# Kernel optimization log

Hardware: AMD Instinct MI355X
Metric: run time of the kernel (lower is better)

The kernel has to match this reference:

```python
import jax, jax.numpy as jnp
import numpy as np

D_MODEL, N_HEADS, D_FF = 1024, 16, 2752
B, S = 2, 2048
EPS = 1e-5


def setup_inputs() -> dict:
    key = jax.random.key(0)
    ks = jax.random.split(key, 8)
    def w(k, fan_in, fan_out):
        std = np.sqrt(2.0 / (fan_in + fan_out))
        return jax.random.truncated_normal(k, -3.0, 3.0, (fan_in, fan_out), jnp.float32) * std
    return {
        "x": jax.random.normal(ks[0], (B, S, D_MODEL), jnp.float32),
        "g1": jnp.ones((D_MODEL,), jnp.float32),
        "g2": jnp.ones((D_MODEL,), jnp.float32),
        "w_q": w(ks[1], D_MODEL, D_MODEL),
        "w_k": w(ks[2], D_MODEL, D_MODEL),
        "w_v": w(ks[3], D_MODEL, D_MODEL),
        "w_o": w(ks[4], D_MODEL, D_MODEL),
        "w1": w(ks[5], D_MODEL, D_FF),
        "w2": w(ks[6], D_FF, D_MODEL),
        "w3": w(ks[7], D_MODEL, D_FF),
    }


def rmsnorm(x, g):
    xf = x.astype(jnp.float32)
    rms = jnp.sqrt(jnp.mean(xf * xf, axis=-1, keepdims=True) + EPS)
    return (xf / rms).astype(x.dtype) * g


def reference(x, g1, g2, w_q, w_k, w_v, w_o, w1, w2, w3):
    b, s, d = x.shape
    h = N_HEADS
    dh = d // h

    # --- causal multi-head self-attention on norm1(x) ---
    xn = rmsnorm(x, g1)
    q = (xn @ w_q).reshape(b, s, h, dh).transpose(0, 2, 1, 3)  # b h s d
    k = (xn @ w_k).reshape(b, s, h, dh).transpose(0, 2, 1, 3)
    v = (xn @ w_v).reshape(b, s, h, dh).transpose(0, 2, 1, 3)

    scores = jnp.einsum('bhqd,bhkd->bhqk', q, k) / jnp.sqrt(jnp.float32(dh))
    causal = jnp.tril(jnp.ones((s, s), dtype=bool))
    scores = jnp.where(causal, scores, -jnp.inf)
    probs = jax.nn.softmax(scores, axis=-1)
    attn = jnp.einsum('bhqk,bhkd->bhqd', probs, v)
    attn = attn.transpose(0, 2, 1, 3).reshape(b, s, d)
    h_res = x + attn @ w_o

    # --- SwiGLU FFN on norm2(h) ---
    hn = rmsnorm(h_res, g2)
    x1 = hn @ w1
    gate = x1 * jax.nn.sigmoid(x1)
    ffn = (gate * (hn @ w3)) @ w2
    return h_res + ffn
```

## Files before the change

kernel.cpp:

```cpp
#include <hip/hip_runtime.h>
#include <hip/hip_bf16.h>

typedef unsigned short u16;
typedef __bf16 bf16x8 __attribute__((ext_vector_type(8)));
typedef float  f32x4  __attribute__((ext_vector_type(4)));

#define D_MODEL 1024
#define SEQ     2048
#define NHEAD   16
#define DHEAD   64
#define QKVS    3072

__device__ __forceinline__ float bflo(unsigned u) { return __uint_as_float(u << 16); }
__device__ __forceinline__ float bfhi(unsigned u) { return __uint_as_float(u & 0xffff0000u); }
__device__ __forceinline__ u16 f2bf(float f) {
    unsigned u = __float_as_uint(f);
    u += 0x7fffu + ((u >> 16) & 1u);
    return (u16)(u >> 16);
}
__device__ __forceinline__ void gld_lds16(const u16* g, u16* l) {
    __builtin_amdgcn_global_load_lds((const __attribute__((address_space(1))) void*)g,
                                     (__attribute__((address_space(3))) void*)l, 16, 0, 0);
}

__global__ void detect_k(const unsigned* __restrict__ g1w, int* __restrict__ flag) {
    int c = 0;
#pragma unroll
    for (int i = 0; i < 8; ++i) c += (g1w[i] == 0x3F800000u) ? 1 : 0;
    *flag = (c >= 4) ? 1 : 0;
}

__global__ __launch_bounds__(256) void tp_k(const void* __restrict__ in_, u16* __restrict__ out,
                                            int K, int N, const int* __restrict__ flagp) {
    __shared__ u16 tile[32][33];
    const int f32 = *flagp;
    int k0 = blockIdx.x * 32, n0 = blockIdx.y * 32;
    int tx = threadIdx.x & 31, ty = threadIdx.x >> 5;
#pragma unroll
    for (int i = 0; i < 32; i += 8) {
        int nn = n0 + tx;
        u16 v = 0;
        if (nn < N) {
            size_t idx = (size_t)(k0 + ty + i) * N + nn;
            v = f32 ? f2bf(((const float*)in_)[idx]) : ((const u16*)in_)[idx];
        }
        tile[ty + i][tx] = v;
    }
    __syncthreads();
#pragma unroll
    for (int i = 0; i < 32; i += 8)
        out[(size_t)(n0 + ty + i) * K + (k0 + tx)] = tile[tx][ty + i];
}

__global__ __launch_bounds__(256) void rms_k(const void* __restrict__ x_, const void* __restrict__ g_,
                                             u16* __restrict__ o, const int* __restrict__ flagp,
                                             int x_raw) {
    const size_t row = blockIdx.x;
    const int f32 = *flagp;
    const int xf32 = f32 & x_raw;
    int t = threadIdx.x;
    float f0, f1, f2, f3, g0, g1, g2, g3;
    if (xf32) {
        float4 xv = *(const float4*)((const float*)x_ + row * D_MODEL + t * 4);
        f0 = xv.x; f1 = xv.y; f2 = xv.z; f3 = xv.w;
    } else {
        uint2 u = *(const uint2*)((const u16*)x_ + row * D_MODEL + t * 4);
        f0 = bflo(u.x); f1 = bfhi(u.x); f2 = bflo(u.y); f3 = bfhi(u.y);
    }
    if (f32) {
        float4 gv = *(const float4*)((const float*)g_ + t * 4);
        g0 = gv.x; g1 = gv.y; g2 = gv.z; g3 = gv.w;
    } else {
        uint2 gu = *(const uint2*)((const u16*)g_ + t * 4);
        g0 = bflo(gu.x); g1 = bfhi(gu.x); g2 = bflo(gu.y); g3 = bfhi(gu.y);
    }
    float s = f0 * f0 + f1 * f1 + f2 * f2 + f3 * f3;
#pragma unroll
    for (int off = 32; off > 0; off >>= 1) s += __shfl_xor(s, off, 64);
    __shared__ float ps[4];
    if ((t & 63) == 0) ps[t >> 6] = s;
    __syncthreads();
    float tot = ps[0] + ps[1] + ps[2] + ps[3];
    float rinv = rsqrtf(tot * (1.0f / D_MODEL) + 1e-5f);
    float fv[4] = {f0, f1, f2, f3};
    float gv2[4] = {g0, g1, g2, g3};
    u16 r[4];
#pragma unroll
    for (int i = 0; i < 4; ++i)
        r[i] = f2bf(fv[i] * rinv * gv2[i]);
    uint2 w;
    w.x = (unsigned)r[0] | ((unsigned)r[1] << 16);
    w.y = (unsigned)r[2] | ((unsigned)r[3] << 16);
    *(uint2*)(o + row * D_MODEL + t * 4) = w;
}

__global__ __launch_bounds__(256) void gemm_k(const u16* __restrict__ A, int lda,
                                              const u16* __restrict__ Bt, int ldb,
                                              u16* C, int ldc,
                                              const void* res, int K, int mode,
                                              const int* __restrict__ flagp, int res_raw,
                                              int out32) {
    __shared__ alignas(16) u16 As[128 * 32];
    __shared__ alignas(16) u16 Bs[128 * 32];
    const int t = threadIdx.x;
    const int rf32 = (mode == 1 && res_raw) ? *flagp : 0;
    const int wid = t >> 6, lane = t & 63;
    const int wm = (wid >> 1) * 64, wn = (wid & 1) * 64;
    const int m0 = blockIdx.x * 128, n0 = blockIdx.y * 128;
    const int fr = lane & 15, quad = lane >> 4;

    f32x4 acc[4][4] = {};

    for (int k0 = 0; k0 < K; k0 += 32) {
        __syncthreads();
#pragma unroll
        for (int r = 0; r < 2; ++r) {
            int e = r * 256 + t;
            int row = e >> 2, c = (e & 3) * 8;
            gld_lds16(A  + (size_t)(m0 + row) * lda + k0 + c, As + e * 8);
            gld_lds16(Bt + (size_t)(n0 + row) * ldb + k0 + c, Bs + e * 8);
        }
        __syncthreads();
        bf16x8 af[4], bfr[4];
#pragma unroll
        for (int i = 0; i < 4; ++i) {
            af[i]  = *(const bf16x8*)(As + (wm + i * 16 + fr) * 32 + quad * 8);
            bfr[i] = *(const bf16x8*)(Bs + (wn + i * 16 + fr) * 32 + quad * 8);
        }
#pragma unroll
        for (int i = 0; i < 4; ++i)
#pragma unroll
            for (int j = 0; j < 4; ++j)
                acc[i][j] = __builtin_amdgcn_mfma_f32_16x16x32_bf16(af[i], bfr[j], acc[i][j], 0, 0, 0);
    }

#pragma unroll
    for (int i = 0; i < 4; ++i)
#pragma unroll
        for (int j = 0; j < 4; ++j)
#pragma unroll
            for (int r2 = 0; r2 < 4; ++r2) {
                int row = m0 + wm + i * 16 + quad * 4 + r2;
                int col = n0 + wn + j * 16 + fr;
                size_t idx = (size_t)row * ldc + col;
                float v = acc[i][j][r2];
                if (mode == 1) {
                    float rv = rf32 ? ((const float*)res)[idx]
                                    : __uint_as_float((unsigned)((const u16*)res)[idx] << 16);
                    v += rv;
                } else if (mode == 2) {
                    float xv = __uint_as_float((unsigned)((const u16*)res)[idx] << 16);
                    xv = fminf(fmaxf(xv, -60.f), 60.f);
                    float sg = xv / (1.0f + __expf(-xv));
                    v = sg * v;
                }
                if (out32) ((float*)C)[idx] = v;
                else       C[idx] = f2bf(v);
            }
}

__global__ __launch_bounds__(256) void vtp_k(const u16* __restrict__ qkv, u16* __restrict__ vt) {
    __shared__ u16 tile[32][33];
    const int bh = blockIdx.z, b = bh >> 4, h = bh & 15;
    const int s0 = blockIdx.x * 32, d0 = blockIdx.y * 32;
    const int tx = threadIdx.x & 31, ty = threadIdx.x >> 5;
#pragma unroll
    for (int i = 0; i < 32; i += 8)
        tile[ty + i][tx] = qkv[(size_t)(b * SEQ + s0 + ty + i) * QKVS + 2048 + h * 64 + d0 + tx];
    __syncthreads();
#pragma unroll
    for (int i = 0; i < 32; i += 8)
        vt[(size_t)(bh * 64 + d0 + ty + i) * SEQ + s0 + tx] = tile[tx][ty + i];
}

#define KPAD 68
#define PPAD 72
__global__ __launch_bounds__(256) void fattn_k(const u16* __restrict__ QKV, const u16* __restrict__ Vt,
                                               u16* __restrict__ O) {
    __shared__ alignas(16) u16 Ks[64 * KPAD];
    __shared__ alignas(16) u16 Vs[64 * KPAD];
    __shared__ alignas(16) u16 Ps[4 * 16 * PPAD];

    const int bh = blockIdx.y;
    const size_t baseqk = ((size_t)(bh >> 4) * SEQ) * QKVS + (size_t)(bh & 15) * DHEAD;
    const size_t baseo  = ((size_t)(bh >> 4) * SEQ) * D_MODEL + (size_t)(bh & 15) * DHEAD;
    const size_t vtbase = (size_t)bh * 64 * SEQ;
    const u16* Qp = QKV + baseqk;
    const u16* Kp = QKV + baseqk + 1024;
    const int chunk = (gridDim.x - 1) - blockIdx.x;
    const int r0 = chunk * 64;
    const int t = threadIdx.x, w = t >> 6, lane = t & 63;
    const int fr = lane & 15, quad = lane >> 4;

    bf16x8 qa[2];
    {
        const u16* qp = Qp + (size_t)(r0 + w * 16 + fr) * QKVS + quad * 8;
        qa[0] = *(const bf16x8*)(qp);
        qa[1] = *(const bf16x8*)(qp + 32);
    }

    f32x4 oacc[4] = {};
    float lp[4] = {};
    u16* Pw = Ps + w * 16 * PPAD;
    const float sc = 0.125f * 1.44269504f;
    const int qrow_base = r0 + w * 16 + quad * 4;

    const int kend = r0 + 64;
    for (int kb = 0; kb < kend; kb += 64) {
        __syncthreads();
#pragma unroll
        for (int it = 0; it < 2; ++it) {
            int e = it * 256 + t;
            int rr = e >> 3, cc = (e & 7) * 8;
            *(uint4*)(Ks + rr * KPAD + cc) = *(const uint4*)(Kp + (size_t)(kb + rr) * QKVS + cc);
            *(uint4*)(Vs + rr * KPAD + cc) = *(const uint4*)(Vt + vtbase + (size_t)rr * SEQ + kb + cc);
        }
        __syncthreads();

        f32x4 sac[4] = {};
#pragma unroll
        for (int n = 0; n < 4; ++n) {
            bf16x8 kf0 = *(const bf16x8*)(Ks + (n * 16 + fr) * KPAD + quad * 8);
            bf16x8 kf1 = *(const bf16x8*)(Ks + (n * 16 + fr) * KPAD + 32 + quad * 8);
            sac[n] = __builtin_amdgcn_mfma_f32_16x16x32_bf16(qa[0], kf0, sac[n], 0, 0, 0);
            sac[n] = __builtin_amdgcn_mfma_f32_16x16x32_bf16(qa[1], kf1, sac[n], 0, 0, 0);
        }
        bf16x8 vf[8];
#pragma unroll
        for (int n = 0; n < 4; ++n) {
            vf[2 * n]     = *(const bf16x8*)(Vs + (n * 16 + fr) * KPAD + quad * 8);
            vf[2 * n + 1] = *(const bf16x8*)(Vs + (n * 16 + fr) * KPAD + 32 + quad * 8);
        }
#pragma unroll
        for (int n = 0; n < 4; ++n) {
            int key = kb + n * 16 + fr;
#pragma unroll
            for (int r = 0; r < 4; ++r) {
                float s = fminf(sac[n][r] * sc, 126.f);
                float p = (key <= qrow_base + r) ? exp2f(s) : 0.f;
                lp[r] += p;
                Pw[(quad * 4 + r) * PPAD + n * 16 + fr] = f2bf(p);
            }
        }
        __threadfence_block();
        bf16x8 pa0 = *(const bf16x8*)(Pw + fr * PPAD + quad * 8);
        bf16x8 pa1 = *(const bf16x8*)(Pw + fr * PPAD + 32 + quad * 8);
#pragma unroll
        for (int n = 0; n < 4; ++n) {
            oacc[n] = __builtin_amdgcn_mfma_f32_16x16x32_bf16(pa0, vf[2 * n],     oacc[n], 0, 0, 0);
            oacc[n] = __builtin_amdgcn_mfma_f32_16x16x32_bf16(pa1, vf[2 * n + 1], oacc[n], 0, 0, 0);
        }
    }

#pragma unroll
    for (int r = 0; r < 4; ++r) {
        float v = lp[r];
        v += __shfl_xor(v, 1, 64);
        v += __shfl_xor(v, 2, 64);
        v += __shfl_xor(v, 4, 64);
        v += __shfl_xor(v, 8, 64);
        lp[r] = 1.0f / v;
    }
#pragma unroll
    for (int r = 0; r < 4; ++r) {
        u16* op = O + baseo + (size_t)(qrow_base + r) * D_MODEL;
#pragma unroll
        for (int n = 0; n < 4; ++n)
            op[n * 16 + fr] = f2bf(oacc[n][r] * lp[r]);
    }
}

extern "C" void kernel_launch(void* const* d_in, const int* in_sizes, int n_in,
                              void* d_out, int out_size, void* d_ws, size_t ws_size,
                              hipStream_t stream) {
    const void* x  = d_in[0];
    const void* g1 = d_in[1];
    const void* g2 = d_in[2];
    const void* wq = d_in[3];
    const void* wk = d_in[4];
    const void* wv = d_in[5];
    const void* wo = d_in[6];
    const void* w1 = d_in[7];
    const void* w2 = d_in[8];
    const void* w3 = d_in[9];
    u16* ws  = (u16*)d_ws;

    u16* xn    = ws;
    u16* qkv   = ws + 4194304;
    u16* x1    = ws + 4194304;
    u16* hres  = ws + 16777216;
    int* flag  = (int*)(ws + 20971520);
    u16* wqkvT = ws + 20971776;
    u16* woT   = ws + 20971776;
    u16* w2T   = ws + 20971776;
    u16* vt    = (u16*)d_out;
    u16* attn  = (u16*)d_out + 4194304;
    u16* w1T   = (u16*)d_out;
    u16* w3T   = (u16*)d_out + 2883584;

    detect_k<<<1, 1, 0, stream>>>((const unsigned*)g1, flag);

    tp_k<<<dim3(32, 32), 256, 0, stream>>>(wq, wqkvT,               1024, 1024, flag);
    tp_k<<<dim3(32, 32), 256, 0, stream>>>(wk, wqkvT + 1048576,     1024, 1024, flag);
    tp_k<<<dim3(32, 32), 256, 0, stream>>>(wv, wqkvT + 2097152,     1024, 1024, flag);
    rms_k<<<4096, 256, 0, stream>>>(x, g1, xn, flag, 1);

    gemm_k<<<dim3(32, 24), 256, 0, stream>>>(xn, 1024, wqkvT, 1024, qkv, QKVS, nullptr, 1024, 0, flag, 0, 0);

    tp_k<<<dim3(32, 32), 256, 0, stream>>>(wo, woT, 1024, 1024, flag);
    vtp_k<<<dim3(64, 2, 32), 256, 0, stream>>>(qkv, vt);
    fattn_k<<<dim3(32, 32), 256, 0, stream>>>(qkv, vt, attn);

    gemm_k<<<dim3(32, 8), 256, 0, stream>>>(attn, 1024, woT, 1024, hres, 1024, x, 1024, 1, flag, 1, 0);

    rms_k<<<4096, 256, 0, stream>>>(hres, g2, xn, flag, 0);

    tp_k<<<dim3(32, 88), 256, 0, stream>>>(w1, w1T, 1024, 2752, flag);
    tp_k<<<dim3(32, 88), 256, 0, stream>>>(w3, w3T, 1024, 2752, flag);
    tp_k<<<dim3(86, 32), 256, 0, stream>>>(w2, w2T, 2752, 1024, flag);

    gemm_k<<<dim3(32, 22), 256, 0, stream>>>(xn, 1024, w1T, 1024, x1, 2816, nullptr, 1024, 0, flag, 0, 0);
    gemm_k<<<dim3(32, 22), 256, 0, stream>>>(xn, 1024, w3T, 1024, x1, 2816, x1, 1024, 2, flag, 0, 0);

    gemm_k<<<dim3(32, 8), 256, 0, stream>>>(x1, 2816, w2T, 2752, (u16*)d_out, 1024, hres, 2752, 1, flag, 0, 1);
}
```

Before: 520.6 us.

## Fuse W1/W3 GEMMs into one SwiGLU kernel and double-buffer attention K/V

Replaces the two FFN GEMM launches (W1, then W3 with SiLU gating in the epilogue) with a single ffn_k kernel. It loads the xn tile once, accumulates both products, and writes the gated result directly, which removes the intermediate x1 write and re-read. The flash attention kernel now double-buffers K/V tiles, prefetching the next block into registers during compute, and skips causal masking on fully unmasked blocks. It also switches P rounding to a cheaper round-half-up conversion. The fused kernel holds two 64-accumulator sets, which raises register pressure, and the attention kernel now uses more LDS.

```diff
diff --git a/kernel.cpp b/kernel.cpp
--- a/kernel.cpp
+++ b/kernel.cpp
@@ -17,6 +17,9 @@
     unsigned u = __float_as_uint(f);
     u += 0x7fffu + ((u >> 16) & 1u);
     return (u16)(u >> 16);
+}
+__device__ __forceinline__ u16 f2bf_fast(float f) {
+    return (u16)((__float_as_uint(f) + 0x8000u) >> 16);
 }
 __device__ __forceinline__ void gld_lds16(const u16* g, u16* l) {
     __builtin_amdgcn_global_load_lds((const __attribute__((address_space(1))) void*)g,
@@ -148,14 +151,67 @@
                     float rv = rf32 ? ((const float*)res)[idx]
                                     : __uint_as_float((unsigned)((const u16*)res)[idx] << 16);
                     v += rv;
-                } else if (mode == 2) {
-                    float xv = __uint_as_float((unsigned)((const u16*)res)[idx] << 16);
-                    xv = fminf(fmaxf(xv, -60.f), 60.f);
-                    float sg = xv / (1.0f + __expf(-xv));
-                    v = sg * v;
                 }
                 if (out32) ((float*)C)[idx] = v;
                 else       C[idx] = f2bf(v);
+            }
+}
+
+__global__ __launch_bounds__(256, 2) void ffn_k(const u16* __restrict__ A,
+                                                const u16* __restrict__ B1t,
+                                                const u16* __restrict__ B3t,
+                                                u16* __restrict__ G, int ldg) {
+    __shared__ alignas(16) u16 As[128 * 32];
+    __shared__ alignas(16) u16 B1s[128 * 32];
+    __shared__ alignas(16) u16 B3s[128 * 32];
+    const int t = threadIdx.x;
+    const int wid = t >> 6, lane = t & 63;
+    const int wm = (wid >> 1) * 64, wn = (wid & 1) * 64;
+    const int m0 = blockIdx.x * 128, n0 = blockIdx.y * 128;
+    const int fr = lane & 15, quad = lane >> 4;
+
+    f32x4 acc1[4][4] = {};
+    f32x4 acc3[4][4] = {};
+
+    for (int k0 = 0; k0 < 1024; k0 += 32) {
+        __syncthreads();
+#pragma unroll
+        for (int r = 0; r < 2; ++r) {
+            int e = r * 256 + t;
+            int row = e >> 2, c = (e & 3) * 8;
+            gld_lds16(A   + (size_t)(m0 + row) * 1024 + k0 + c, As  + e * 8);
+            gld_lds16(B1t + (size_t)(n0 + row) * 1024 + k0 + c, B1s + e * 8);
+            gld_lds16(B3t + (size_t)(n0 + row) * 1024 + k0 + c, B3s + e * 8);
+        }
+        __syncthreads();
+        bf16x8 af[4], b1[4], b3[4];
+#pragma unroll
+        for (int i = 0; i < 4; ++i) {
+            af[i] = *(const bf16x8*)(As  + (wm + i * 16 + fr) * 32 + quad * 8);
+            b1[i] = *(const bf16x8*)(B1s + (wn + i * 16 + fr) * 32 + quad * 8);
+            b3[i] = *(const bf16x8*)(B3s + (wn + i * 16 + fr) * 32 + quad * 8);
+        }
+#pragma unroll
+        for (int i = 0; i < 4; ++i)
+#pragma unroll
+            for (int j = 0; j < 4; ++j) {
+                acc1[i][j] = __builtin_amdgcn_mfma_f32_16x16x32_bf16(af[i], b1[j], acc1[i][j], 0, 0, 0);
+                acc3[i][j] = __builtin_amdgcn_mfma_f32_16x16x32_bf16(af[i], b3[j], acc3[i][j], 0, 0, 0);
+            }
+    }
+
+#pragma unroll
+    for (int i = 0; i < 4; ++i)
+#pragma unroll
+        for (int j = 0; j < 4; ++j)
+#pragma unroll
+            for (int r2 = 0; r2 < 4; ++r2) {
+                int row = m0 + wm + i * 16 + quad * 4 + r2;
+                int col = n0 + wn + j * 16 + fr;
+                float xv = acc1[i][j][r2];
+                xv = fminf(fmaxf(xv, -60.f), 60.f);
+                float sg = xv / (1.0f + __expf(-xv));
+                G[(size_t)row * ldg + col] = f2bf(sg * acc3[i][j][r2]);
             }
 }
 
@@ -177,8 +233,8 @@
 #define PPAD 72
 __global__ __launch_bounds__(256) void fattn_k(const u16* __restrict__ QKV, const u16* __restrict__ Vt,
                                                u16* __restrict__ O) {
-    __shared__ alignas(16) u16 Ks[64 * KPAD];
-    __shared__ alignas(16) u16 Vs[64 * KPAD];
+    __shared__ alignas(16) u16 Ks[2][64 * KPAD];
+    __shared__ alignas(16) u16 Vs[2][64 * KPAD];
     __shared__ alignas(16) u16 Ps[4 * 16 * PPAD];
 
     const int bh = blockIdx.y;
@@ -191,6 +247,8 @@
     const int r0 = chunk * 64;
     const int t = threadIdx.x, w = t >> 6, lane = t & 63;
     const int fr = lane & 15, quad = lane >> 4;
+    const int rr0 = t >> 3, cc0 = (t & 7) * 8;
+    const int rr1 = rr0 + 32;
 
     bf16x8 qa[2];
     {
@@ -203,43 +261,63 @@
     float lp[4] = {};
     u16* Pw = Ps + w * 16 * PPAD;
     const float sc = 0.125f * 1.44269504f;
-    const int qrow_base = r0 + w * 16 + quad * 4;
-
+    const int qrow_min  = r0 + w * 16;
+    const int qrow_base = qrow_min + quad * 4;
     const int kend = r0 + 64;
-    for (int kb = 0; kb < kend; kb += 64) {
-        __syncthreads();
-#pragma unroll
-        for (int it = 0; it < 2; ++it) {
-            int e = it * 256 + t;
-            int rr = e >> 3, cc = (e & 7) * 8;
-            *(uint4*)(Ks + rr * KPAD + cc) = *(const uint4*)(Kp + (size_t)(kb + rr) * QKVS + cc);
-            *(uint4*)(Vs + rr * KPAD + cc) = *(const uint4*)(Vt + vtbase + (size_t)rr * SEQ + kb + cc);
-        }
-        __syncthreads();
-
+
+    {
+        uint4 k0v = *(const uint4*)(Kp + (size_t)rr0 * QKVS + cc0);
+        uint4 k1v = *(const uint4*)(Kp + (size_t)rr1 * QKVS + cc0);
+        uint4 v0v = *(const uint4*)(Vt + vtbase + (size_t)rr0 * SEQ + cc0);
+        uint4 v1v = *(const uint4*)(Vt + vtbase + (size_t)rr1 * SEQ + cc0);
+        *(uint4*)(Ks[0] + rr0 * KPAD + cc0) = k0v;
+        *(uint4*)(Ks[0] + rr1 * KPAD + cc0) = k1v;
+        *(uint4*)(Vs[0] + rr0 * KPAD + cc0) = v0v;
+        *(uint4*)(Vs[0] + rr1 * KPAD + cc0) = v1v;
+    }
+    __syncthreads();
+
+    int cur = 0;
+    for (int kb = 0; kb < kend; kb += 64, cur ^= 1) {
+        const int nxt = kb + 64;
+        const bool have = nxt < kend;
+        uint4 kn0, kn1, vn0, vn1;
+        if (have) {
+            kn0 = *(const uint4*)(Kp + (size_t)(nxt + rr0) * QKVS + cc0);
+            kn1 = *(const uint4*)(Kp + (size_t)(nxt + rr1) * QKVS + cc0);
+            vn0 = *(const uint4*)(Vt + vtbase + (size_t)rr0 * SEQ + nxt + cc0);
+            vn1 = *(const uint4*)(Vt + vtbase + (size_t)rr1 * SEQ + nxt + cc0);
+        }
+
+        const u16* Kc = Ks[cur];
+        const u16* Vc = Vs[cur];
         f32x4 sac[4] = {};
 #pragma unroll
         for (int n = 0; n < 4; ++n) {
-            bf16x8 kf0 = *(const bf16x8*)(Ks + (n * 16 + fr) * KPAD + quad * 8);
-            bf16x8 kf1 = *(const bf16x8*)(Ks + (n * 16 + fr) * KPAD + 32 + quad * 8);
+            bf16x8 kf0 = *(const bf16x8*)(Kc + (n * 16 + fr) * KPAD + quad * 8);
+            bf16x8 kf1 = *(const bf16x8*)(Kc + (n * 16 + fr) * KPAD + 32 + quad * 8);
             sac[n] = __builtin_amdgcn_mfma_f32_16x16x32_bf16(qa[0], kf0, sac[n], 0, 0, 0);
             sac[n] = __builtin_amdgcn_mfma_f32_16x16x32_bf16(qa[1], kf1, sac[n], 0, 0, 0);
         }
-        bf16x8 vf[8];
-#pragma unroll
-        for (int n = 0; n < 4; ++n) {
-            vf[2 * n]     = *(const bf16x8*)(Vs + (n * 16 + fr) * KPAD + quad * 8);
-            vf[2 * n + 1] = *(const bf16x8*)(Vs + (n * 16 + fr) * KPAD + 32 + quad * 8);
-        }
-#pragma unroll
-        for (int n = 0; n < 4; ++n) {
-            int key = kb + n * 16 + fr;
-#pragma unroll
-            for (int r = 0; r < 4; ++r) {
-                float s = fminf(sac[n][r] * sc, 126.f);
-                float p = (key <= qrow_base + r) ? exp2f(s) : 0.f;
-                lp[r] += p;
-                Pw[(quad * 4 + r) * PPAD + n * 16 + fr] = f2bf(p);
+        if (nxt <= qrow_min) {
+#pragma unroll
+            for (int n = 0; n < 4; ++n)
+#pragma unroll
+                for (int r = 0; r < 4; ++r) {
+                    float p = exp2f(fminf(sac[n][r] * sc, 126.f));
+                    lp[r] += p;
+                    Pw[(quad * 4 + r) * PPAD + n * 16 + fr] = f2bf_fast(p);
+                }
+        } else {
+#pragma unroll
+            for (int n = 0; n < 4; ++n) {
+                int key = kb + n * 16 + fr;
+#pragma unroll
+                for (int r = 0; r < 4; ++r) {
+                    float p = (key <= qrow_base + r) ? exp2f(fminf(sac[n][r] * sc, 126.f)) : 0.f;
+                    lp[r] += p;
+                    Pw[(quad * 4 + r) * PPAD + n * 16 + fr] = f2bf_fast(p);
+                }
             }
         }
         __threadfence_block();
@@ -247,8 +325,19 @@
         bf16x8 pa1 = *(const bf16x8*)(Pw + fr * PPAD + 32 + quad * 8);
 #pragma unroll
         for (int n = 0; n < 4; ++n) {
-            oacc[n] = __builtin_amdgcn_mfma_f32_16x16x32_bf16(pa0, vf[2 * n],     oacc[n], 0, 0, 0);
-            oacc[n] = __builtin_amdgcn_mfma_f32_16x16x32_bf16(pa1, vf[2 * n + 1], oacc[n], 0, 0, 0);
+            bf16x8 vf0 = *(const bf16x8*)(Vc + (n * 16 + fr) * KPAD + quad * 8);
+            bf16x8 vf1 = *(const bf16x8*)(Vc + (n * 16 + fr) * KPAD + 32 + quad * 8);
+            oacc[n] = __builtin_amdgcn_mfma_f32_16x16x32_bf16(pa0, vf0, oacc[n], 0, 0, 0);
+            oacc[n] = __builtin_amdgcn_mfma_f32_16x16x32_bf16(pa1, vf1, oacc[n], 0, 0, 0);
+        }
+
+        if (have) {
+            int nb = cur ^ 1;
+            *(uint4*)(Ks[nb] + rr0 * KPAD + cc0) = kn0;
+            *(uint4*)(Ks[nb] + rr1 * KPAD + cc0) = kn1;
+            *(uint4*)(Vs[nb] + rr0 * KPAD + cc0) = vn0;
+            *(uint4*)(Vs[nb] + rr1 * KPAD + cc0) = vn1;
+            __syncthreads();
         }
     }
 
@@ -287,7 +376,7 @@
 
     u16* xn    = ws;
     u16* qkv   = ws + 4194304;
-    u16* x1    = ws + 4194304;
+    u16* gate  = ws + 4194304;
     u16* hres  = ws + 16777216;
     int* flag  = (int*)(ws + 20971520);
     u16* wqkvT = ws + 20971776;
@@ -300,9 +389,9 @@
 
     detect_k<<<1, 1, 0, stream>>>((const unsigned*)g1, flag);
 
-    tp_k<<<dim3(32, 32), 256, 0, stream>>>(wq, wqkvT,               1024, 1024, flag);
-    tp_k<<<dim3(32, 32), 256, 0, stream>>>(wk, wqkvT + 1048576,     1024, 1024, flag);
-    tp_k<<<dim3(32, 32), 256, 0, stream>>>(wv, wqkvT + 2097152,     1024, 1024, flag);
+    tp_k<<<dim3(32, 32), 256, 0, stream>>>(wq, wqkvT,           1024, 1024, flag);
+    tp_k<<<dim3(32, 32), 256, 0, stream>>>(wk, wqkvT + 1048576, 1024, 1024, flag);
+    tp_k<<<dim3(32, 32), 256, 0, stream>>>(wv, wqkvT + 2097152, 1024, 1024, flag);
     rms_k<<<4096, 256, 0, stream>>>(x, g1, xn, flag, 1);
 
     gemm_k<<<dim3(32, 24), 256, 0, stream>>>(xn, 1024, wqkvT, 1024, qkv, QKVS, nullptr, 1024, 0, flag, 0, 0);
@@ -319,8 +408,7 @@
     tp_k<<<dim3(32, 88), 256, 0, stream>>>(w3, w3T, 1024, 2752, flag);
     tp_k<<<dim3(86, 32), 256, 0, stream>>>(w2, w2T, 2752, 1024, flag);
 
-    gemm_k<<<dim3(32, 22), 256, 0, stream>>>(xn, 1024, w1T, 1024, x1, 2816, nullptr, 1024, 0, flag, 0, 0);
-    gemm_k<<<dim3(32, 22), 256, 0, stream>>>(xn, 1024, w3T, 1024, x1, 2816, x1, 1024, 2, flag, 0, 0);
-
-    gemm_k<<<dim3(32, 8), 256, 0, stream>>>(x1, 2816, w2T, 2752, (u16*)d_out, 1024, hres, 2752, 1, flag, 0, 1);
-}
+    ffn_k<<<dim3(32, 22), 256, 0, stream>>>(xn, w1T, w3T, gate, 2816);
+
+    gemm_k<<<dim3(32, 8), 256, 0, stream>>>(gate, 2816, w2T, 2752, (u16*)d_out, 1024, hres, 2752, 1, flag, 0, 1);
+}
```

Result: slower. 652.3 us (+25.3%).
